# Kernel optimization log

Measured on AMD Instinct MI355X. Metric: run time of the kernel, lower is better.

## Reference

```python
import jax, jax.numpy as jnp
import numpy as np

MASK_PENALTY = 1e15  # matches the TF module's additive mask constant


def setup_inputs() -> dict:
    key = jax.random.key(0)
    k1, k2, k3, k4, k5 = jax.random.split(key, 5)
    B, S, E, DK, DV = 4, 2048, 1024, 128, 128
    inputs = jax.random.normal(k1, (B, S, E), dtype=jnp.float32)
    mask = jax.random.randint(k2, (B, S, S), 0, 2, dtype=jnp.int32)
    # Dense kernels (glorot-ish scale)
    Wq = jax.random.normal(k3, (E, DK), dtype=jnp.float32) / np.float32(np.sqrt(E))
    Wk = jax.random.normal(k4, (E, DK), dtype=jnp.float32) / np.float32(np.sqrt(E))
    Wv = jax.random.normal(k5, (E, DV), dtype=jnp.float32) / np.float32(np.sqrt(E))
    return {"inputs": inputs, "mask": mask, "Wq": Wq, "Wk": Wk, "Wv": Wv}


def reference(inputs, mask, Wq, Wk, Wv):
    # q, k, v projections (no bias)
    q = jnp.einsum("bse,ed->bsd", inputs, Wq)  # [B,S,DK]
    k = jnp.einsum("bse,ed->bsd", inputs, Wk)  # [B,S,DK]
    v = jnp.einsum("bse,ed->bsd", inputs, Wv)  # [B,S,DV]
    dim_k = Wq.shape[-1]
    scale = jnp.asarray(1.0 / np.sqrt(dim_k), dtype=q.dtype)
    dot_p = jnp.einsum("bqd,bkd->bqk", q, k) * scale  # [B,S,S]
    dot_p = dot_p - MASK_PENALTY * mask.astype(dot_p.dtype)
    softm = jax.nn.softmax(dot_p, axis=-1)
    return jnp.einsum("bqk,bkd->bqd", softm, v)  # [B,S,DV]
```

## Files before the change

kernel.cpp:

```cpp
#include <hip/hip_runtime.h>
#include <stdint.h>


#define SEQ   2048
#define EDIM  1024
#define DDIM  128
#define QS2   0.1275174329f

typedef unsigned short u16;
typedef unsigned int   u32;
using short8 = __attribute__((ext_vector_type(8))) short;
using f32x4  = __attribute__((ext_vector_type(4))) float;
using int4v  = __attribute__((ext_vector_type(4))) int;
using u32x2  = __attribute__((ext_vector_type(2))) unsigned int;

__device__ __forceinline__ u16 f2bf(float x) {
    uint32_t u = __float_as_uint(x);
    return (u16)((u + 0x7fffu + ((u >> 16) & 1u)) >> 16);
}
__device__ __forceinline__ float ex2(float x) {
    float r; asm("v_exp_f32 %0, %1" : "=v"(r) : "v"(x)); return r;
}

__device__ __forceinline__ void gld16(const void* gsrc, void* lds_dst) {
    __builtin_amdgcn_global_load_lds(
        (const __attribute__((address_space(1))) uint32_t*)(uintptr_t)gsrc,
        (__attribute__((address_space(3))) uint32_t*)(uint32_t)(uintptr_t)lds_dst,
        16, 0, 0);
}

__global__ __launch_bounds__(256) void prep_kernel(
    const float* __restrict__ Wq, const float* __restrict__ Wk, const float* __restrict__ Wv,
    u16* __restrict__ Wt)
{
    __shared__ u16 tl[64][65];
    const int t = blockIdx.x;
    const int tid = threadIdx.x;
    const int wsel = t >> 5;
    const int tile = t & 31;
    const int k0 = (tile >> 1) * 64;
    const int n0 = (tile & 1) * 64;
    const float* W = (wsel == 0) ? Wq : ((wsel == 1) ? Wk : Wv);
#pragma unroll
    for (int it = 0; it < 16; ++it) {
        const int idx = it * 256 + tid;
        const int r = idx >> 6, c = idx & 63;
        tl[c][r] = f2bf(W[(size_t)(k0 + r) * DDIM + n0 + c]);
    }
    __syncthreads();
    u16* Wtp = Wt + (size_t)wsel * DDIM * EDIM;
#pragma unroll
    for (int it = 0; it < 16; ++it) {
        const int idx = it * 256 + tid;
        const int r = idx >> 6, c = idx & 63;
        Wtp[(size_t)(n0 + r) * EDIM + k0 + c] = tl[r][c];
    }
}

__global__ __launch_bounds__(512, 1) void proj_kernel(
    const float* __restrict__ Ain, const u16* __restrict__ Wtb,
    u16* __restrict__ Qb, u16* __restrict__ Kb, u16* __restrict__ Vtb)
{
    __shared__ __align__(16) uint8_t smem[106496];
    const int tid = threadIdx.x;
    const int w = tid >> 6, lane = tid & 63;
    const int lq = lane & 15, lg = lane >> 4;

    const int bid = blockIdx.x;
    const int wg = (bid & 7) * 32 + (bid >> 3);
    const int m0 = wg * 32;

    f32x4 acc[2][3] = {};

    auto stageP = [&](int buf, int kt) {
        const int k0 = kt * 64;
        uint8_t* wtb = smem + 8192 + buf * 49152;
#pragma unroll
        for (int i = 0; i < 6; ++i) {
            const int G = i * 512 + tid;
            const int n = G >> 3, c = G & 7;
            gld16(Wtb + (size_t)n * EDIM + k0 + ((c ^ (n & 7)) << 3),
                  wtb + i * 8192 + w * 1024);
        }
        const int row = tid >> 4, c4 = tid & 15;
        const int c2 = c4 >> 1, h = c4 & 1;
        const float* s2 = Ain + (size_t)(m0 + row) * EDIM + k0 + c2 * 8 + h * 4;
        const f32x4 a0 = *(const f32x4*)s2;
        u32x2 pk;
        pk[0] = (u32)f2bf(a0[0]) | ((u32)f2bf(a0[1]) << 16);
        pk[1] = (u32)f2bf(a0[2]) | ((u32)f2bf(a0[3]) << 16);
        *(u32x2*)(smem + buf * 4096 + row * 128 + ((c2 ^ (row & 7)) << 4) + h * 8) = pk;
    };

    stageP(0, 0);
    __syncthreads();

#pragma unroll 1
    for (int kt = 0; kt < 16; ++kt) {
        const int cur = kt & 1;
        if (kt < 15) stageP(cur ^ 1, kt + 1);
        const uint8_t* abase = smem + cur * 4096;
        const uint8_t* wbase = smem + 8192 + cur * 49152;
        __builtin_amdgcn_s_setprio(1);
#pragma unroll
        for (int ks = 0; ks < 2; ++ks) {
            short8 af[2];
#pragma unroll
            for (int mf = 0; mf < 2; ++mf) {
                const int arow = mf * 16 + lq;
                af[mf] = *(const short8*)(abase + arow * 128 + ((((ks << 2) + lg) ^ (arow & 7)) << 4));
            }
#pragma unroll
            for (int j = 0; j < 3; ++j) {
                const int brow = (w + j * 8) * 16 + lq;
                const short8 bf = *(const short8*)(wbase + brow * 128 + ((((ks << 2) + lg) ^ (brow & 7)) << 4));
#pragma unroll
                for (int mf = 0; mf < 2; ++mf)
                    acc[mf][j] = __builtin_amdgcn_mfma_f32_16x16x32_bf16(af[mf], bf, acc[mf][j], 0, 0, 0);
            }
        }
        __builtin_amdgcn_s_setprio(0);
        __syncthreads();
    }

#pragma unroll
    for (int mf = 0; mf < 2; ++mf)
#pragma unroll
        for (int r = 0; r < 4; ++r) {
            const int mrow = mf * 16 + lg * 4 + r;
            const int n = w * 16 + lq;
            *(u16*)(smem + mrow * 256 + (((n >> 3) ^ (mrow & 7)) << 4) + ((n & 7) << 1))
                = f2bf(acc[mf][0][r] * QS2);
            *(u16*)(smem + 8192 + mrow * 256 + (((n >> 3) ^ (mrow & 7)) << 4) + ((n & 7) << 1))
                = f2bf(acc[mf][1][r]);
            const int d = n, s = mrow;
            *(u16*)(smem + 16384 + d * 64 + (((s >> 3) ^ (d & 3)) << 4) + ((s & 7) << 1))
                = f2bf(acc[mf][2][r]);
        }
    __syncthreads();
    {
        const int b = m0 >> 11, s0b = m0 & 2047;
        const int mm2 = tid >> 4, gp = tid & 15;
        const int n0 = (gp ^ (mm2 & 7)) * 8;
        const short8 vq = *(const short8*)(smem + mm2 * 256 + (gp << 4));
        *(short8*)(Qb + (size_t)(m0 + mm2) * 128 + n0) = vq;
        const short8 vk = *(const short8*)(smem + 8192 + mm2 * 256 + (gp << 4));
        *(short8*)(Kb + (size_t)(m0 + mm2) * 128 + n0) = vk;
        const int d = tid >> 2, cg = tid & 3;
        const int sg = cg ^ (d & 3);
        const short8 vv = *(const short8*)(smem + 16384 + d * 64 + (cg << 4));
        *(short8*)(Vtb + (size_t)b * DDIM * SEQ + (size_t)d * SEQ + s0b + sg * 8) = vv;
    }
}

__global__ __launch_bounds__(512, 1) void flash_kernel(
    const int* __restrict__ mask,
    const u16* __restrict__ Qb, const u16* __restrict__ Kb, const u16* __restrict__ Vtb,
    float* __restrict__ out)
{
    __shared__ __align__(16) uint8_t smem[139264];
    __shared__ u32 mlds[2112];
    __shared__ float ml_m[2][4][16], ml_l[2][4][16], recipL[32];

    const int tid = threadIdx.x;
    const int w = tid >> 6, lane = tid & 63;
    const int qi = w >> 2, ki = w & 3;
    const int lq = lane & 15, lg = lane >> 4;

    const int bid = blockIdx.x;
    const int qt = (bid & 7) * 32 + (bid >> 3);
    const int b = qt >> 6;
    const int q0 = (qt & 63) << 5;
    const size_t qrow0 = (size_t)b * SEQ + q0;

    const u16* Qp = Qb + (qrow0 + qi * 16) * 128;
    const u16* Kp = Kb + (size_t)b * SEQ * 128;
    const u16* Vp = Vtb + (size_t)b * DDIM * SEQ;

    uint8_t* kvb0 = smem + ki * 32768;
    uint8_t* pbase = smem + 131072 + w * 1024;

    auto stage = [&](uint8_t* kvb, int kv0) {
        if (qi == 0) {
#pragma unroll
            for (int i = 0; i < 8; ++i) {
                const int G = i * 64 + lane;
                const int row = G >> 4, c = G & 15;
                gld16(Kp + (size_t)(kv0 + row) * 128 + ((c ^ (row & 7)) << 3),
                      kvb + i * 1024);
            }
        } else {
#pragma unroll
            for (int i = 0; i < 8; ++i) {
                const int G = i * 64 + lane;
                const int dd = G >> 2, c = G & 3;
                gld16(Vp + (size_t)dd * SEQ + kv0 + ((c ^ ((dd ^ (dd >> 2)) & 3)) << 3),
                      kvb + 8192 + i * 1024);
            }
        }
    };

    stage(kvb0, ki * 512);
    short8 qf[4];
#pragma unroll
    for (int ks = 0; ks < 4; ++ks)
        qf[ks] = *(const short8*)(Qp + (size_t)lq * 128 + ks * 32 + lg * 8);
    {
        const int r = tid >> 4, c0 = (tid & 15) * 4;
        const int* srcm = mask + (qrow0 + r) * (size_t)SEQ + (size_t)c0 * 32;
#pragma unroll
        for (int j = 0; j < 4; ++j) {
            u32 bits = 0;
#pragma unroll
            for (int it = 0; it < 8; ++it) {
                const int4v v = *(const int4v*)(srcm + j * 32 + it * 4);
                bits |= (v[0] != 0 ? 1u : 0u) << (it * 4 + 0);
                bits |= (v[1] != 0 ? 1u : 0u) << (it * 4 + 1);
                bits |= (v[2] != 0 ? 1u : 0u) << (it * 4 + 2);
                bits |= (v[3] != 0 ? 1u : 0u) << (it * 4 + 3);
            }
            mlds[r * 66 + c0 + j] = bits;
        }
    }
    __syncthreads();

    f32x4 acc[8] = {};
    float m = -1e30f, l = 0.0f;
    const int mbidx = (qi * 16 + lq) * 66 + ki * 16;

#pragma unroll 1
    for (int t = 0; t < 16; ++t) {
        uint8_t* kvb = kvb0 + (t & 1) * 16384;
        if (t < 15) stage(kvb0 + ((t + 1) & 1) * 16384, ki * 512 + (t + 1) * 32);
        const u32 mw = mlds[mbidx + t];
        __builtin_amdgcn_sched_barrier(0);

        f32x4 sacc[2] = {};
        __builtin_amdgcn_s_setprio(1);
#pragma unroll
        for (int ks = 0; ks < 4; ++ks)
#pragma unroll
            for (int nf = 0; nf < 2; ++nf) {
                const int krow = nf * 16 + lq;
                const short8 kf = *(const short8*)(kvb + krow * 256 + ((((ks << 2) + lg) ^ (krow & 7)) << 4));
                sacc[nf] = __builtin_amdgcn_mfma_f32_16x16x32_bf16(kf, qf[ks], sacc[nf], 0, 0, 0);
            }
        __builtin_amdgcn_s_setprio(0);

        float sv[2][4];
#pragma unroll
        for (int nf = 0; nf < 2; ++nf)
#pragma unroll
            for (int r = 0; r < 4; ++r)
                sv[nf][r] = sacc[nf][r] + (((mw >> (nf * 16 + lg * 4 + r)) & 1u) ? -1e15f : 0.0f);
        float tm = sv[0][0];
#pragma unroll
        for (int nf = 0; nf < 2; ++nf)
#pragma unroll
            for (int r = 0; r < 4; ++r) tm = fmaxf(tm, sv[nf][r]);
        tm = fmaxf(tm, __shfl_xor(tm, 16));
        tm = fmaxf(tm, __shfl_xor(tm, 32));
        if (!__all(tm <= m + 13.0f)) {
            const float mnew = fmaxf(m, tm);
            const float sf = ex2(m - mnew);
            m = mnew;
            l *= sf;
#pragma unroll
            for (int df = 0; df < 8; ++df) acc[df] *= sf;
        }
        float p[2][4];
        float rs = 0.0f;
#pragma unroll
        for (int nf = 0; nf < 2; ++nf)
#pragma unroll
            for (int r = 0; r < 4; ++r) { p[nf][r] = ex2(sv[nf][r] - m); rs += p[nf][r]; }
        rs += __shfl_xor(rs, 16);
        rs += __shfl_xor(rs, 32);
        l += rs;

#pragma unroll
        for (int nf = 0; nf < 2; ++nf)
#pragma unroll
            for (int h = 0; h < 2; ++h) {
                u32 pk;
                asm("v_cvt_pk_bf16_f32 %0, %1, %2" : "=v"(pk) : "v"(p[nf][2 * h]), "v"(p[nf][2 * h + 1]));
                const int kv = nf * 16 + lg * 4 + 2 * h;
                *(u32*)(pbase + lq * 64 + (((kv >> 3) ^ (lq & 3)) << 4) + ((kv << 1) & 15)) = pk;
            }
        const short8 pf = *(const short8*)(pbase + lq * 64 + ((lg ^ (lq & 3)) << 4));

        __builtin_amdgcn_s_setprio(1);
#pragma unroll
        for (int df = 0; df < 8; ++df) {
            const int dd = df * 16 + lq;
            const short8 vf = *(const short8*)(kvb + 8192 + dd * 64 + ((lg ^ ((dd ^ (dd >> 2)) & 3)) << 4));
            acc[df] = __builtin_amdgcn_mfma_f32_16x16x32_bf16(vf, pf, acc[df], 0, 0, 0);
        }
        __builtin_amdgcn_s_setprio(0);

        asm volatile("s_waitcnt vmcnt(0)" ::: "memory");
        __builtin_amdgcn_s_barrier();
    }

    if (lg == 0) { ml_m[qi][ki][lq] = m; ml_l[qi][ki][lq] = l; }
    __syncthreads();
    {
        const float m0v = ml_m[qi][0][lq], m1v = ml_m[qi][1][lq];
        const float m2v = ml_m[qi][2][lq], m3v = ml_m[qi][3][lq];
        const float mm = fmaxf(fmaxf(m0v, m1v), fmaxf(m2v, m3v));
        const float Lg = ml_l[qi][0][lq] * ex2(m0v - mm) + ml_l[qi][1][lq] * ex2(m1v - mm)
                       + ml_l[qi][2][lq] * ex2(m2v - mm) + ml_l[qi][3][lq] * ex2(m3v - mm);
        if (ki == 0 && lg == 0) recipL[qi * 16 + lq] = 1.0f / Lg;
        const float s = ex2(m - mm);
        float* Ol = (float*)smem;
        float* dstq = Ol + ((size_t)(qi * 4 + ki) * 16 + lq) * 132;
#pragma unroll
        for (int df = 0; df < 8; ++df) {
            const f32x4 vsc = acc[df] * s;
            *(f32x4*)(dstq + df * 16 + lg * 4) = vsc;
        }
    }
    __syncthreads();
    {
        const float* Ol = (const float*)smem;
        const int row = tid >> 4, c0 = (tid & 15) * 8;
        const int rqi = row >> 4, rq = row & 15;
        const float rl = recipL[row];
        f32x4 s0 = {}, s1 = {};
#pragma unroll
        for (int kk = 0; kk < 4; ++kk) {
            const float* p2 = Ol + ((size_t)(rqi * 4 + kk) * 16 + rq) * 132 + c0;
            s0 += *(const f32x4*)p2;
            s1 += *(const f32x4*)(p2 + 4);
        }
        s0 *= rl; s1 *= rl;
        float* op = out + (qrow0 + row) * 128 + c0;
        *(f32x4*)op = s0;
        *(f32x4*)(op + 4) = s1;
    }
}

extern "C" void kernel_launch(void* const* d_in, const int* in_sizes, int n_in,
                              void* d_out, int out_size, void* d_ws, size_t ws_size,
                              hipStream_t stream) {
    (void)in_sizes; (void)n_in; (void)out_size; (void)ws_size;
    const float* inputs = (const float*)d_in[0];
    const int*   mask   = (const int*)d_in[1];
    const float* Wq     = (const float*)d_in[2];
    const float* Wk     = (const float*)d_in[3];
    const float* Wv     = (const float*)d_in[4];
    float* out = (float*)d_out;

    uint8_t* ws = (uint8_t*)d_ws;
    u16* Wtb = (u16*)ws;
    u16* Qb  = (u16*)(ws + 786432);
    u16* Kb  = (u16*)(ws + 2883584);
    u16* Vtb = (u16*)(ws + 4980736);

    hipLaunchKernelGGL(prep_kernel, dim3(96), dim3(256), 0, stream, Wq, Wk, Wv, Wtb);
    hipLaunchKernelGGL(proj_kernel, dim3(256), dim3(512), 0, stream, inputs, Wtb, Qb, Kb, Vtb);
    hipLaunchKernelGGL(flash_kernel, dim3(256), dim3(512), 0, stream, mask, Qb, Kb, Vtb, out);
}
```

Baseline: 174.8 us.

## Split flash attention KV range across two blocks, precompute mask bits, add reduce

Mask bit-packing moves out of the flash kernel into the prep kernel, which now spans 2048 extra blocks writing a packed bitmask to workspace. The flash kernel splits each query tile's KV range into two halves (512 blocks instead of 256), shrinks LDS to a single K/V buffer so more blocks can be resident, and writes partial outputs with their max and sum. A new reduce kernel combines the two halves. The aim is better occupancy and parallelism and less mask-conversion work on the critical path. The cost is the loss of double-buffered prefetch (loads now sit between barriers), extra partial-output traffic and one more launch.

```diff
diff --git a/kernel.cpp b/kernel.cpp
--- a/kernel.cpp
+++ b/kernel.cpp
@@ -30,30 +30,51 @@
 }
 
 __global__ __launch_bounds__(256) void prep_kernel(
+    const int* __restrict__ mask,
     const float* __restrict__ Wq, const float* __restrict__ Wk, const float* __restrict__ Wv,
-    u16* __restrict__ Wt)
+    u32* __restrict__ Mbits, u16* __restrict__ Wt)
 {
+    __shared__ u32 nib32[2048];
     __shared__ u16 tl[64][65];
-    const int t = blockIdx.x;
+    const int bx = blockIdx.x;
     const int tid = threadIdx.x;
-    const int wsel = t >> 5;
-    const int tile = t & 31;
-    const int k0 = (tile >> 1) * 64;
-    const int n0 = (tile & 1) * 64;
-    const float* W = (wsel == 0) ? Wq : ((wsel == 1) ? Wk : Wv);
-#pragma unroll
-    for (int it = 0; it < 16; ++it) {
-        const int idx = it * 256 + tid;
-        const int r = idx >> 6, c = idx & 63;
-        tl[c][r] = f2bf(W[(size_t)(k0 + r) * DDIM + n0 + c]);
-    }
-    __syncthreads();
-    u16* Wtp = Wt + (size_t)wsel * DDIM * EDIM;
-#pragma unroll
-    for (int it = 0; it < 16; ++it) {
-        const int idx = it * 256 + tid;
-        const int r = idx >> 6, c = idx & 63;
-        Wtp[(size_t)(n0 + r) * EDIM + k0 + c] = tl[r][c];
+    if (bx < 2048) {
+        const int* src = mask + (size_t)bx * 8192;
+#pragma unroll
+        for (int it = 0; it < 8; ++it) {
+            const int idx = it * 256 + tid;
+            const int4v v = *(const int4v*)(src + idx * 4);
+            const u32 nb = (v[0] != 0 ? 1u : 0u) | (v[1] != 0 ? 2u : 0u)
+                         | (v[2] != 0 ? 4u : 0u) | (v[3] != 0 ? 8u : 0u);
+            nib32[(idx & 7) * 256 + ((idx >> 3) ^ ((idx & 7) << 2))] = nb;
+        }
+        __syncthreads();
+        u32 word = 0;
+#pragma unroll
+        for (int j = 0; j < 8; ++j)
+            word |= (nib32[j * 256 + (tid ^ (j << 2))] & 0xFu) << (4 * j);
+        Mbits[bx * 256 + tid] = word;
+    } else {
+        const int t = bx - 2048;
+        const int wsel = t >> 5;
+        const int tile = t & 31;
+        const int k0 = (tile >> 1) * 64;
+        const int n0 = (tile & 1) * 64;
+        const float* W = (wsel == 0) ? Wq : ((wsel == 1) ? Wk : Wv);
+#pragma unroll
+        for (int it = 0; it < 16; ++it) {
+            const int idx = it * 256 + tid;
+            const int r = idx >> 6, c = idx & 63;
+            tl[c][r] = f2bf(W[(size_t)(k0 + r) * DDIM + n0 + c]);
+        }
+        __syncthreads();
+        u16* Wtp = Wt + (size_t)wsel * DDIM * EDIM;
+#pragma unroll
+        for (int it = 0; it < 16; ++it) {
+            const int idx = it * 256 + tid;
+            const int r = idx >> 6, c = idx & 63;
+            Wtp[(size_t)(n0 + r) * EDIM + k0 + c] = tl[r][c];
+        }
     }
 }
 
@@ -153,14 +174,13 @@
     }
 }
 
-__global__ __launch_bounds__(512, 1) void flash_kernel(
-    const int* __restrict__ mask,
+__global__ __launch_bounds__(512, 4) void flash_kernel(
+    const u32* __restrict__ Mb,
     const u16* __restrict__ Qb, const u16* __restrict__ Kb, const u16* __restrict__ Vtb,
-    float* __restrict__ out)
+    float* __restrict__ Opart, float* __restrict__ Mpart, float* __restrict__ Lpart)
 {
-    __shared__ __align__(16) uint8_t smem[139264];
-    __shared__ u32 mlds[2112];
-    __shared__ float ml_m[2][4][16], ml_l[2][4][16], recipL[32];
+    __shared__ __align__(16) uint8_t smem[73728];
+    __shared__ float ml_m[2][4][16], ml_l[2][4][16];
 
     const int tid = threadIdx.x;
     const int w = tid >> 6, lane = tid & 63;
@@ -168,7 +188,9 @@
     const int lq = lane & 15, lg = lane >> 4;
 
     const int bid = blockIdx.x;
-    const int qt = (bid & 7) * 32 + (bid >> 3);
+    const int u = bid >> 3, xcd = bid & 7;
+    const int qt = xcd * 32 + (u & 31);
+    const int h = u >> 5;
     const int b = qt >> 6;
     const int q0 = (qt & 63) << 5;
     const size_t qrow0 = (size_t)b * SEQ + q0;
@@ -176,65 +198,44 @@
     const u16* Qp = Qb + (qrow0 + qi * 16) * 128;
     const u16* Kp = Kb + (size_t)b * SEQ * 128;
     const u16* Vp = Vtb + (size_t)b * DDIM * SEQ;
-
-    uint8_t* kvb0 = smem + ki * 32768;
-    uint8_t* pbase = smem + 131072 + w * 1024;
-
-    auto stage = [&](uint8_t* kvb, int kv0) {
-        if (qi == 0) {
-#pragma unroll
-            for (int i = 0; i < 8; ++i) {
-                const int G = i * 64 + lane;
-                const int row = G >> 4, c = G & 15;
-                gld16(Kp + (size_t)(kv0 + row) * 128 + ((c ^ (row & 7)) << 3),
-                      kvb + i * 1024);
-            }
-        } else {
-#pragma unroll
-            for (int i = 0; i < 8; ++i) {
-                const int G = i * 64 + lane;
-                const int dd = G >> 2, c = G & 3;
-                gld16(Vp + (size_t)dd * SEQ + kv0 + ((c ^ ((dd ^ (dd >> 2)) & 3)) << 3),
-                      kvb + 8192 + i * 1024);
-            }
+    const u32* mrp = Mb + (qrow0 + qi * 16 + lq) * 64 + h * 32 + ki * 8;
+
+    const int kv00 = h * 1024 + ki * 256;
+    uint8_t* kvb = smem + ki * 16384;
+    uint8_t* pbase = smem + 65536 + w * 1024;
+
+    auto stageK = [&](int kv0) {
+#pragma unroll
+        for (int i = 0; i < 8; ++i) {
+            const int G = i * 64 + lane;
+            const int row = G >> 4, c = G & 15;
+            gld16(Kp + (size_t)(kv0 + row) * 128 + ((c ^ (row & 7)) << 3),
+                  kvb + i * 1024);
         }
     };
-
-    stage(kvb0, ki * 512);
+    auto stageV = [&](int kv0) {
+#pragma unroll
+        for (int i = 0; i < 8; ++i) {
+            const int G = i * 64 + lane;
+            const int dd = G >> 2, c = G & 3;
+            gld16(Vp + (size_t)dd * SEQ + kv0 + ((c ^ ((dd ^ (dd >> 2)) & 3)) << 3),
+                  kvb + 8192 + i * 1024);
+        }
+    };
+
+    if (qi == 0) stageK(kv00); else stageV(kv00);
     short8 qf[4];
 #pragma unroll
     for (int ks = 0; ks < 4; ++ks)
         qf[ks] = *(const short8*)(Qp + (size_t)lq * 128 + ks * 32 + lg * 8);
-    {
-        const int r = tid >> 4, c0 = (tid & 15) * 4;
-        const int* srcm = mask + (qrow0 + r) * (size_t)SEQ + (size_t)c0 * 32;
-#pragma unroll
-        for (int j = 0; j < 4; ++j) {
-            u32 bits = 0;
-#pragma unroll
-            for (int it = 0; it < 8; ++it) {
-                const int4v v = *(const int4v*)(srcm + j * 32 + it * 4);
-                bits |= (v[0] != 0 ? 1u : 0u) << (it * 4 + 0);
-                bits |= (v[1] != 0 ? 1u : 0u) << (it * 4 + 1);
-                bits |= (v[2] != 0 ? 1u : 0u) << (it * 4 + 2);
-                bits |= (v[3] != 0 ? 1u : 0u) << (it * 4 + 3);
-            }
-            mlds[r * 66 + c0 + j] = bits;
-        }
-    }
+    u32 mw = mrp[0];
     __syncthreads();
 
     f32x4 acc[8] = {};
     float m = -1e30f, l = 0.0f;
-    const int mbidx = (qi * 16 + lq) * 66 + ki * 16;
 
 #pragma unroll 1
-    for (int t = 0; t < 16; ++t) {
-        uint8_t* kvb = kvb0 + (t & 1) * 16384;
-        if (t < 15) stage(kvb0 + ((t + 1) & 1) * 16384, ki * 512 + (t + 1) * 32);
-        const u32 mw = mlds[mbidx + t];
-        __builtin_amdgcn_sched_barrier(0);
-
+    for (int t = 0; t < 8; ++t) {
         f32x4 sacc[2] = {};
         __builtin_amdgcn_s_setprio(1);
 #pragma unroll
@@ -246,6 +247,8 @@
                 sacc[nf] = __builtin_amdgcn_mfma_f32_16x16x32_bf16(kf, qf[ks], sacc[nf], 0, 0, 0);
             }
         __builtin_amdgcn_s_setprio(0);
+        __syncthreads();
+        if (qi == 0 && t < 7) stageK(kv00 + (t + 1) * 32);
 
         float sv[2][4];
 #pragma unroll
@@ -281,10 +284,10 @@
 #pragma unroll
         for (int nf = 0; nf < 2; ++nf)
 #pragma unroll
-            for (int h = 0; h < 2; ++h) {
+            for (int hh = 0; hh < 2; ++hh) {
                 u32 pk;
-                asm("v_cvt_pk_bf16_f32 %0, %1, %2" : "=v"(pk) : "v"(p[nf][2 * h]), "v"(p[nf][2 * h + 1]));
-                const int kv = nf * 16 + lg * 4 + 2 * h;
+                asm("v_cvt_pk_bf16_f32 %0, %1, %2" : "=v"(pk) : "v"(p[nf][2 * hh]), "v"(p[nf][2 * hh + 1]));
+                const int kv = nf * 16 + lg * 4 + 2 * hh;
                 *(u32*)(pbase + lq * 64 + (((kv >> 3) ^ (lq & 3)) << 4) + ((kv << 1) & 15)) = pk;
             }
         const short8 pf = *(const short8*)(pbase + lq * 64 + ((lg ^ (lq & 3)) << 4));
@@ -297,9 +300,11 @@
             acc[df] = __builtin_amdgcn_mfma_f32_16x16x32_bf16(vf, pf, acc[df], 0, 0, 0);
         }
         __builtin_amdgcn_s_setprio(0);
-
-        asm volatile("s_waitcnt vmcnt(0)" ::: "memory");
-        __builtin_amdgcn_s_barrier();
+        __syncthreads();
+        if (qi == 1 && t < 7) stageV(kv00 + (t + 1) * 32);
+        const u32 mwn = (t < 7) ? mrp[t + 1] : 0u;
+        __syncthreads();
+        mw = mwn;
     }
 
     if (lg == 0) { ml_m[qi][ki][lq] = m; ml_l[qi][ki][lq] = l; }
@@ -310,7 +315,10 @@
         const float mm = fmaxf(fmaxf(m0v, m1v), fmaxf(m2v, m3v));
         const float Lg = ml_l[qi][0][lq] * ex2(m0v - mm) + ml_l[qi][1][lq] * ex2(m1v - mm)
                        + ml_l[qi][2][lq] * ex2(m2v - mm) + ml_l[qi][3][lq] * ex2(m3v - mm);
-        if (ki == 0 && lg == 0) recipL[qi * 16 + lq] = 1.0f / Lg;
+        if (ki == 0 && lg == 0) {
+            Mpart[h * 8192 + qrow0 + qi * 16 + lq] = mm;
+            Lpart[h * 8192 + qrow0 + qi * 16 + lq] = Lg;
+        }
         const float s = ex2(m - mm);
         float* Ol = (float*)smem;
         float* dstq = Ol + ((size_t)(qi * 4 + ki) * 16 + lq) * 132;
@@ -325,7 +333,6 @@
         const float* Ol = (const float*)smem;
         const int row = tid >> 4, c0 = (tid & 15) * 8;
         const int rqi = row >> 4, rq = row & 15;
-        const float rl = recipL[row];
         f32x4 s0 = {}, s1 = {};
 #pragma unroll
         for (int kk = 0; kk < 4; ++kk) {
@@ -333,11 +340,29 @@
             s0 += *(const f32x4*)p2;
             s1 += *(const f32x4*)(p2 + 4);
         }
-        s0 *= rl; s1 *= rl;
-        float* op = out + (qrow0 + row) * 128 + c0;
+        float* op = Opart + ((size_t)(h * 8192) + qrow0 + row) * 128 + c0;
         *(f32x4*)op = s0;
         *(f32x4*)(op + 4) = s1;
     }
+}
+
+__global__ __launch_bounds__(256) void reduce_kernel(
+    const float* __restrict__ Op, const float* __restrict__ Mp,
+    const float* __restrict__ Lp, float* __restrict__ out)
+{
+    const int row = blockIdx.x * 16 + (threadIdx.x >> 4);
+    const int c0 = (threadIdx.x & 15) * 8;
+    const float m0 = Mp[row], m1 = Mp[8192 + row];
+    const float l0 = Lp[row], l1 = Lp[8192 + row];
+    const float M = fmaxf(m0, m1);
+    const float e0 = ex2(m0 - M), e1 = ex2(m1 - M);
+    const float rl = 1.0f / (l0 * e0 + l1 * e1);
+    const float* p0 = Op + (size_t)row * 128 + c0;
+    const float* p1 = Op + (size_t)(8192 + row) * 128 + c0;
+    f32x4 a0 = *(const f32x4*)p0 * e0 + *(const f32x4*)p1 * e1;
+    f32x4 a1 = *(const f32x4*)(p0 + 4) * e0 + *(const f32x4*)(p1 + 4) * e1;
+    *(f32x4*)(out + (size_t)row * 128 + c0) = a0 * rl;
+    *(f32x4*)(out + (size_t)row * 128 + c0 + 4) = a1 * rl;
 }
 
 extern "C" void kernel_launch(void* const* d_in, const int* in_sizes, int n_in,
@@ -352,12 +377,17 @@
     float* out = (float*)d_out;
 
     uint8_t* ws = (uint8_t*)d_ws;
-    u16* Wtb = (u16*)ws;
-    u16* Qb  = (u16*)(ws + 786432);
-    u16* Kb  = (u16*)(ws + 2883584);
-    u16* Vtb = (u16*)(ws + 4980736);
-
-    hipLaunchKernelGGL(prep_kernel, dim3(96), dim3(256), 0, stream, Wq, Wk, Wv, Wtb);
+    u16*   Wtb   = (u16*)ws;
+    u16*   Qb    = (u16*)(ws + 786432);
+    u16*   Kb    = (u16*)(ws + 2883584);
+    u16*   Vtb   = (u16*)(ws + 4980736);
+    u32*   Mbits = (u32*)(ws + 7077888);
+    float* Opart = (float*)(ws + 9175040);
+    float* Mpart = (float*)(ws + 17563648);
+    float* Lpart = (float*)(ws + 17629184);
+
+    hipLaunchKernelGGL(prep_kernel, dim3(2144), dim3(256), 0, stream, mask, Wq, Wk, Wv, Mbits, Wtb);
     hipLaunchKernelGGL(proj_kernel, dim3(256), dim3(512), 0, stream, inputs, Wtb, Qb, Kb, Vtb);
-    hipLaunchKernelGGL(flash_kernel, dim3(256), dim3(512), 0, stream, mask, Qb, Kb, Vtb, out);
-}
+    hipLaunchKernelGGL(flash_kernel, dim3(512), dim3(512), 0, stream, Mbits, Qb, Kb, Vtb, Opart, Mpart, Lpart);
+    hipLaunchKernelGGL(reduce_kernel, dim3(512), dim3(256), 0, stream, Opart, Mpart, Lpart, out);
+}
```

Measured after the change: 171.3 us. -2.0%, faster.
